# Kernel optimization log

Hardware: AMD Instinct MI355X
Metric: run time of the kernel (lower is better)

Reference implementation:

```python
import jax, jax.numpy as jnp
from jax import lax
import numpy as np

KERNEL = 3      # patch kernel
RATE = 2        # dilation / downscale rate
SCALE = 10.0    # softmax_scale
EPS = 1e-4


def extract_patches(x, k, s):
    """TF tf.image.extract_patches with SAME padding.
    x: [B,H,W,C] -> [B, oh, ow, k, k, C] with (ky,kx,c) ordering like TF depth."""
    B, H, W, C = x.shape
    oh, ow = -(-H // s), -(-W // s)
    ph = max((oh - 1) * s + k - H, 0)
    pw = max((ow - 1) * s + k - W, 0)
    xp = jnp.pad(x, ((0, 0), (ph // 2, ph - ph // 2), (pw // 2, pw - pw // 2), (0, 0)))
    rows = []
    for ky in range(k):
        cols = [xp[:, ky: ky + (oh - 1) * s + 1: s, kx: kx + (ow - 1) * s + 1: s, :]
                for kx in range(k)]
        rows.append(jnp.stack(cols, axis=3))        # [B,oh,ow,kx,C]
    return jnp.stack(rows, axis=3)                  # [B,oh,ow,ky,kx,C]


def resize_half(x):
    B, H, W, C = x.shape
    return jax.image.resize(x, (B, H // 2, W // 2, C), 'bilinear', antialias=False)


def fuse_diag(a):
    """conv2d of [N,N] image with eye(3) kernel (SAME): out[i,j]=a[i-1,j-1]+a[i,j]+a[i+1,j+1]."""
    p = jnp.pad(a, 1)
    return p[:-2, :-2] + p[1:-1, 1:-1] + p[2:, 2:]


def setup_inputs() -> dict:
    key = jax.random.key(0)
    x = jax.random.normal(key, (4, 96, 96, 128), jnp.float32)
    # binary mask with a central square hole (1 = missing region)
    mask = jnp.zeros((4, 96, 96, 1), jnp.float32).at[:, 24:72, 24:72, :].set(1.0)
    return {"x": x, "mask": mask}


def reference(x, mask):
    B, H, W, C = x.shape
    k, rate = KERNEL, RATE

    # raw patches from full-res x, stride rate -> deconv weights
    raw_p = extract_patches(x, k, rate)                     # [B,h,w,k,k,C]
    h, w = raw_p.shape[1], raw_p.shape[2]
    L = h * w
    raw_w = raw_p.reshape(B, L, k, k, C).transpose(0, 2, 3, 4, 1)   # [B,k,k,C,L]

    # downscaled foreground/background (f == b in this module) and mask
    f = resize_half(x)                                      # [B,h,w,C]
    m = resize_half(mask)                                   # [B,h,w,1]

    wp = extract_patches(f, k, 1).reshape(B, L, k, k, C).transpose(0, 2, 3, 4, 1)  # [B,k,k,C,L]
    mp = extract_patches(m, k, 1).reshape(B, L, -1)         # [B,L,k*k*1]
    mm = (jnp.mean(mp, axis=-1) == 0.0).astype(x.dtype)     # [B,L] valid-patch mask

    fp = extract_patches(f, k, 1)                           # [B,h,w,k,k,C] query patches

    def per_sample(fp_i, wi, raw_wi, mm_i):
        # normalized cross-correlation: conv2d(f_i, wi_normed, SAME)
        norm = jnp.maximum(jnp.sqrt(jnp.sum(wi * wi, axis=(0, 1, 2))), EPS)   # [L]
        wn = wi / norm
        yi = jnp.einsum('hwabc,abcl->hwl', fp_i, wn)        # [h,w,L]

        # diagonal fuse (eye(3) conv) on both patch-grid orderings
        a = fuse_diag(yi.reshape(L, L))
        a = a.reshape(h, w, h, w).transpose(1, 0, 3, 2).reshape(L, L)
        a = fuse_diag(a)
        a = a.reshape(w, h, w, h).transpose(1, 0, 3, 2)     # [h,w,h,w]
        yi = a.reshape(h, w, L)

        # masked softmax over source patches
        yi = yi * mm_i
        yi = jax.nn.softmax(yi * SCALE, axis=-1) * mm_i

        # conv2d_transpose(yi, raw_wi, [1,H,W,C], strides=rate) == vjp of strided conv
        def fwd(z):  # z: [H,W,C] -> [h,w,L]
            return lax.conv_general_dilated(z[None], raw_wi, (rate, rate), 'SAME',
                                            dimension_numbers=('NHWC', 'HWIO', 'NHWC'))[0]
        _, vjp = jax.vjp(fwd, jnp.zeros((H, W, C), x.dtype))
        return vjp(yi)[0] / (rate * rate)                   # [H,W,C]

    return jax.vmap(per_sample)(fp, wp, raw_w, mm)          # [B,H,W,C]
```

## Files before the change

kernel.cpp:

```cpp
#include <hip/hip_runtime.h>
#include <hip/hip_fp16.h>
#include <stdint.h>
#include <string.h>


namespace {

constexpr int B_ = 4;
constexpr int H_ = 96;
constexpr int W_ = 96;
constexpr int C_ = 128;
constexpr int h_ = 48;
constexpr int L_ = 2304;
constexpr int N9_ = 1152;
constexpr int K3_ = 384;
constexpr float SCALE_ = 10.0f;
constexpr float EPS_ = 1e-4f;

constexpr int OUT_F16 = 1;
constexpr int OUT_BF16 = 2;

typedef unsigned short u16;
typedef __attribute__((ext_vector_type(8))) short bfrag8;
typedef __attribute__((ext_vector_type(8))) unsigned short ushort8;
typedef __attribute__((ext_vector_type(4))) float f32x4;
typedef __attribute__((ext_vector_type(2))) float f32x2;

__device__ __forceinline__ u16 f2bf(float f) {
  uint32_t x;
  __builtin_memcpy(&x, &f, 4);
  uint32_t lsb = (x >> 16) & 1u;
  x += 0x7fffu + lsb;
  return (u16)(x >> 16);
}
__device__ __forceinline__ float bf2f(u16 u) {
  uint32_t v = ((uint32_t)u) << 16;
  float f;
  __builtin_memcpy(&f, &v, 4);
  return f;
}
__device__ __forceinline__ u16 f2h(float f) {
  __half h = __float2half(f);
  u16 u;
  __builtin_memcpy(&u, &h, 2);
  return u;
}
__device__ __forceinline__ float h2f(u16 u) {
  __half h;
  __builtin_memcpy(&h, &u, 2);
  return __half2float(h);
}

__device__ __forceinline__ void gload16(const u16* g, void* l) {
  __builtin_amdgcn_global_load_lds(
      (const __attribute__((address_space(1))) void*)g,
      (__attribute__((address_space(3))) void*)l, 16, 0, 0);
}

__device__ __forceinline__ int xcd_swz8(int orig, int nwg) {
  int q = nwg >> 3, r = nwg & 7;
  int xcd = orig & 7, pos = orig >> 3;
  return (xcd < r ? xcd * (q + 1) : r * (q + 1) + (xcd - r) * q) + pos;
}

__device__ __forceinline__ uint32_t swzb(uint32_t byte) {
  return byte ^ (((byte >> 7) & 7u) << 4);
}

__global__ __launch_bounds__(128) void k_down(const float* __restrict__ x,
                                              u16* __restrict__ F3a,
                                              u16* __restrict__ F3b,
                                              float* __restrict__ S) {
  int blk = blockIdx.x;
  int b = blk / L_, l = blk % L_;
  int p = l / h_, q = l % h_;
  int c = threadIdx.x;
  const float* xb = x + (((size_t)b * H_ + 2 * p) * W_ + 2 * q) * C_ + c;
  float v = 0.25f * (xb[0] + xb[C_] + xb[(size_t)W_ * C_] + xb[(size_t)W_ * C_ + C_]);
  u16 hi = f2bf(v);
  u16 lo = f2bf(v - bf2f(hi));
  size_t base = ((size_t)b * L_ + l) * K3_;
  F3a[base + c] = hi; F3a[base + 128 + c] = hi; F3a[base + 256 + c] = lo;
  F3b[base + c] = hi; F3b[base + 128 + c] = lo; F3b[base + 256 + c] = hi;
  float ss = v * v;
#pragma unroll
  for (int o = 32; o >= 1; o >>= 1) ss += __shfl_xor(ss, o, 64);
  __shared__ float w2[2];
  if ((c & 63) == 0) w2[c >> 6] = ss;
  __syncthreads();
  if (c == 0) S[(size_t)b * L_ + l] = w2[0] + w2[1];
}

__global__ __launch_bounds__(256) void k_mask(const float* __restrict__ mask,
                                              float* __restrict__ md) {
  int i = blockIdx.x * 256 + threadIdx.x;
  int b = i / L_, l = i % L_, p = l / h_, q = l % h_;
  const float* mb = mask + ((size_t)b * H_ + 2 * p) * W_ + 2 * q;
  md[i] = 0.25f * (mb[0] + mb[1] + mb[W_] + mb[W_ + 1]);
}

__global__ __launch_bounds__(256) void k_mmnorm(const float* __restrict__ S,
                                                const float* __restrict__ md,
                                                float* __restrict__ mm,
                                                float* __restrict__ ninv) {
  int i = blockIdx.x * 256 + threadIdx.x;
  int b = i / L_, l = i % L_, p = l / h_, q = l % h_;
  float ssum = 0.f, msum = 0.f;
#pragma unroll
  for (int a = 0; a < 3; a++) {
    int rp = p - 1 + a;
#pragma unroll
    for (int bb = 0; bb < 3; bb++) {
      int rq = q - 1 + bb;
      bool ok = ((unsigned)rp < (unsigned)h_) && ((unsigned)rq < (unsigned)h_);
      int idx = ok ? (b * L_ + rp * h_ + rq) : 0;
      float sv = S[idx], mv = md[idx];
      if (ok) { ssum += sv; msum += mv; }
    }
  }
  mm[i] = (msum == 0.f) ? 1.f : 0.f;
  float n = fmaxf(sqrtf(ssum), EPS_);
  ninv[i] = 1.f / n;
}

__global__ __launch_bounds__(256) void k_xpack(const float* __restrict__ x,
                                               u16* __restrict__ XpT) {
  int lt = blockIdx.x * 32, jt = blockIdx.y * 64, bz = blockIdx.z;
  __shared__ u16 tile[32][65];
  int t = threadIdx.x;
  int jj = t & 63, lq = t >> 6;
  for (int pass = 0; pass < 8; ++pass) {
    int ll = pass * 4 + lq;
    int l = lt + ll;
    int p = l / h_, q = l % h_;
    int j = jt + jj;
    int a = j / 384, rem = j % 384, bb = rem / 128, c = rem % 128;
    int gy = 2 * p + a, gx = 2 * q + bb;
    float v = 0.f;
    if (gy < H_ && gx < W_) v = x[(((size_t)bz * H_ + gy) * W_ + gx) * C_ + c];
    tile[ll][jj] = f2bf(v);
  }
  __syncthreads();
  int lw = t & 31, jq = t >> 5;
  for (int pass = 0; pass < 8; ++pass) {
    int j2 = pass * 8 + jq;
    XpT[((size_t)bz * N9_ + jt + j2) * L_ + lt + lw] = tile[lw][j2];
  }
}

template <int OUT>
__global__ __launch_bounds__(256) void gemm_bt(const u16* __restrict__ A,
                                               const u16* __restrict__ B,
                                               void* __restrict__ Cv,
                                               int N, int Kd,
                                               size_t sA, size_t sB, size_t sC) {
  const u16* Ab = A + (size_t)blockIdx.z * sA;
  const u16* Bb = B + (size_t)blockIdx.z * sB;
  int nwg = gridDim.x * gridDim.y;
  int orig = blockIdx.y * gridDim.x + blockIdx.x;
  int wgid = xcd_swz8(orig, nwg);
  int bx = wgid % gridDim.x, by = wgid / gridDim.x;
  int m0 = by * 128, n0 = bx * 128;

  __shared__ char As[2][8192];
  __shared__ char Bs[2][8192];
  int t = threadIdx.x;
  int lane = t & 63, wv = t >> 6, wr = wv >> 1, wc = wv & 1;
  int mrow = lane & 15, kg = lane >> 4;
  f32x4 acc[4][4];
#pragma unroll
  for (int i = 0; i < 4; i++)
#pragma unroll
    for (int j = 0; j < 4; j++) acc[i][j] = (f32x4)(0.0f);

  uint32_t d16 = (uint32_t)t * 16u;
  uint32_t sz = swzb(d16);
  int rowp = (int)(sz >> 6);
  int kcp = (int)((sz >> 4) & 3u);
  const u16* ga0 = Ab + (size_t)(m0 + rowp) * Kd + kcp * 8;
  const u16* ga1 = Ab + (size_t)(m0 + 64 + rowp) * Kd + kcp * 8;
  const u16* gb0 = Bb + (size_t)(n0 + rowp) * Kd + kcp * 8;
  const u16* gb1 = Bb + (size_t)(n0 + 64 + rowp) * Kd + kcp * 8;

  auto STAGE = [&](int buf, int k0) {
    gload16(ga0 + k0, As[buf] + wv * 1024);
    gload16(ga1 + k0, As[buf] + 4096 + wv * 1024);
    gload16(gb0 + k0, Bs[buf] + wv * 1024);
    gload16(gb1 + k0, Bs[buf] + 4096 + wv * 1024);
  };

  int nsteps = Kd >> 5;
  STAGE(0, 0);
  __syncthreads();
  int cur = 0;
  for (int s = 0; s < nsteps; ++s) {
    if (s + 1 < nsteps) STAGE(cur ^ 1, (s + 1) << 5);
    bfrag8 af[4], bf[4];
#pragma unroll
    for (int i = 0; i < 4; i++) {
      uint32_t byte = (uint32_t)(wr * 64 + i * 16 + mrow) * 64u + (uint32_t)kg * 16u;
      af[i] = *(const bfrag8*)(As[cur] + swzb(byte));
    }
#pragma unroll
    for (int i = 0; i < 4; i++) {
      uint32_t byte = (uint32_t)(wc * 64 + i * 16 + mrow) * 64u + (uint32_t)kg * 16u;
      bf[i] = *(const bfrag8*)(Bs[cur] + swzb(byte));
    }
#pragma unroll
    for (int i = 0; i < 4; i++)
#pragma unroll
      for (int j = 0; j < 4; j++)
        acc[i][j] = __builtin_amdgcn_mfma_f32_16x16x32_bf16(af[i], bf[j], acc[i][j], 0, 0, 0);
    __syncthreads();
    cur ^= 1;
  }
#pragma unroll
  for (int i = 0; i < 4; i++)
#pragma unroll
    for (int j = 0; j < 4; j++)
#pragma unroll
      for (int r = 0; r < 4; r++) {
        int gr = m0 + wr * 64 + i * 16 + kg * 4 + r;
        int gc = n0 + wc * 64 + j * 16 + mrow;
        if (OUT == OUT_BF16) {
          ((u16*)Cv)[(size_t)blockIdx.z * sC + (size_t)gr * N + gc] = f2bf(acc[i][j][r]);
        } else {
          ((u16*)Cv)[(size_t)blockIdx.z * sC + (size_t)gr * N + gc] = f2h(acc[i][j][r]);
        }
      }
}

template <int S>
__device__ __forceinline__ void tap(const u16* __restrict__ Ub, int o8, bool tok,
                                    const bool* md, int b, float* acc) {
  constexpr int REM = ((S % 8) + 8) % 8;
  int off = tok ? (o8 + S * 2305) : (8 + REM);
  float v[8];
  if constexpr (REM == 0) {
    ushort8 w = *(const ushort8*)(Ub + off);
#pragma unroll
    for (int i = 0; i < 8; i++) v[i] = h2f(w[i]);
  } else if constexpr (REM == 1) {
    ushort8 w = *(const ushort8*)(Ub + off - 1);
    u16 sc = Ub[off + 7];
#pragma unroll
    for (int i = 0; i < 7; i++) v[i] = h2f(w[i + 1]);
    v[7] = h2f(sc);
  } else {
    u16 sc = Ub[off];
    ushort8 w = *(const ushort8*)(Ub + off + 1);
    v[0] = h2f(sc);
#pragma unroll
    for (int i = 1; i < 8; i++) v[i] = h2f(w[i - 1]);
  }
#pragma unroll
  for (int i = 0; i < 8; i++) acc[i] += (tok && md[b + i]) ? v[i] : 0.f;
}

__global__ __launch_bounds__(256) void k_patchsum(const u16* __restrict__ U,
                                                  u16* __restrict__ V,
                                                  const float* __restrict__ ninv,
                                                  int b0) {
  int blk = xcd_swz8(blockIdx.x, gridDim.x);
  int bz = blockIdx.z;
  int o8 = (blk * 256 + (int)threadIdx.x) * 8;
  int R = o8 / L_;
  int col = o8 - R * L_;
  const u16* Ub = U + (size_t)bz * L_ * L_;
  u16* Vb = V + (size_t)bz * L_ * L_;
  int hq = R / h_, wq = R % h_, ps = col / h_, qs0 = col % h_;
  bool ra[3], rb[3], ca[3];
#pragma unroll
  for (int a = 0; a < 3; a++) {
    ra[a] = (unsigned)(hq - 1 + a) < (unsigned)h_;
    rb[a] = (unsigned)(wq - 1 + a) < (unsigned)h_;
    ca[a] = (unsigned)(ps - 1 + a) < (unsigned)h_;
  }
  bool md[10];
#pragma unroll
  for (int d = 0; d < 10; d++) md[d] = (unsigned)(qs0 - 1 + d) < (unsigned)h_;

  float acc[8];
#pragma unroll
  for (int i = 0; i < 8; i++) acc[i] = 0.f;

  bool t0 = ra[0] && ca[0];
  bool t1 = ra[1] && ca[1];
  bool t2 = ra[2] && ca[2];
  tap<-49>(Ub, o8, t0 && rb[0], md, 0, acc);
  tap<-48>(Ub, o8, t0 && rb[1], md, 1, acc);
  tap<-47>(Ub, o8, t0 && rb[2], md, 2, acc);
  tap<-1>(Ub, o8, t1 && rb[0], md, 0, acc);
  tap<0>(Ub, o8, t1 && rb[1], md, 1, acc);
  tap<1>(Ub, o8, t1 && rb[2], md, 2, acc);
  tap<47>(Ub, o8, t2 && rb[0], md, 0, acc);
  tap<48>(Ub, o8, t2 && rb[1], md, 1, acc);
  tap<49>(Ub, o8, t2 && rb[2], md, 2, acc);

  const float* nvb = ninv + (size_t)(b0 + bz) * L_ + col;
  ushort8 ov;
#pragma unroll
  for (int i = 0; i < 8; i++) ov[i] = f2h(acc[i] * nvb[i]);
  *(ushort8*)(Vb + o8) = ov;
}

__global__ __launch_bounds__(256) void k_fsm(const u16* __restrict__ V1,
                                             const float* __restrict__ mm,
                                             u16* __restrict__ Aout,
                                             int b0) {
  int i = xcd_swz8(blockIdx.x, L_), bz = blockIdx.y;
  int hq = i / h_, wq = i % h_;
  const u16* Vb = V1 + (size_t)bz * L_ * L_;
  const float* mmb = mm + (size_t)(b0 + bz) * L_;
  u16* arow = Aout + ((size_t)bz * L_ + i) * L_;
  int t = threadIdx.x;

  uint32_t rowBase[3];
  bool rw0[3], rw1[3], rw2[3];
#pragma unroll
  for (int d2 = 0; d2 < 3; d2++) {
    int TA = wq * h_ + hq + (d2 - 1);
    bool ok = (TA >= 0) && (TA < L_);
    int TAc = ok ? TA : 0;
    int iB = (TAc % h_) * h_ + TAc / h_;
    rowBase[d2] = (uint32_t)(iB * L_);
    rw0[d2] = ok && (iB - 1 >= 0);
    rw1[d2] = ok;
    rw2[d2] = ok && (iB + 1 < L_);
  }

  int jy = t / h_, jx = t % h_;
  float y[9];
  float mx = -3.0e38f;
#pragma unroll
  for (int cc = 0; cc < 9; cc++) {
    int j = cc * 256 + t;
    int jB0 = (jy >= 1) ? (j - h_) : (j + (L_ - h_ - 1));
    int jB1 = j;
    int jB2 = (jy <= h_ - 2) ? (j + h_) : (j - (L_ - h_ - 1));
    bool tb0 = (j > 0), tb2 = (j < L_ - 1);
    float s = 0.f;
    {
      uint32_t oc = rowBase[0] + (uint32_t)jB0;
      bool w0 = rw0[0] && tb0 && (jB0 > 0);
      bool w1 = rw1[0] && tb0;
      bool w2 = rw2[0] && tb0 && (jB0 < L_ - 1);
      float vm = h2f(Vb[w0 ? oc - (L_ + 1) : 0u]);
      float vc = h2f(Vb[w1 ? oc : 0u]);
      float vp = h2f(Vb[w2 ? oc + (L_ + 1) : 0u]);
      s += (w0 ? vm : 0.f) + (w1 ? vc : 0.f) + (w2 ? vp : 0.f);
    }
    {
      uint32_t oc = rowBase[1] + (uint32_t)jB1;
      bool w0 = rw0[1] && (jB1 > 0);
      bool w1 = rw1[1];
      bool w2 = rw2[1] && (jB1 < L_ - 1);
      float vm = h2f(Vb[w0 ? oc - (L_ + 1) : 0u]);
      float vc = h2f(Vb[w1 ? oc : 0u]);
      float vp = h2f(Vb[w2 ? oc + (L_ + 1) : 0u]);
      s += (w0 ? vm : 0.f) + (w1 ? vc : 0.f) + (w2 ? vp : 0.f);
    }
    {
      uint32_t oc = rowBase[2] + (uint32_t)jB2;
      bool w0 = rw0[2] && tb2 && (jB2 > 0);
      bool w1 = rw1[2] && tb2;
      bool w2 = rw2[2] && tb2 && (jB2 < L_ - 1);
      float vm = h2f(Vb[w0 ? oc - (L_ + 1) : 0u]);
      float vc = h2f(Vb[w1 ? oc : 0u]);
      float vp = h2f(Vb[w2 ? oc + (L_ + 1) : 0u]);
      s += (w0 ? vm : 0.f) + (w1 ? vc : 0.f) + (w2 ? vp : 0.f);
    }
    float zv = s * mmb[j] * SCALE_;
    y[cc] = zv;
    mx = fmaxf(mx, zv);
    jx += 256 - 5 * h_;
    jy += 5;
    if (jx >= h_) { jx -= h_; jy += 1; }
  }

  int lane = t & 63, wid = t >> 6;
  __shared__ float wredm[4];
  __shared__ float wreds[4];
#pragma unroll
  for (int o = 32; o >= 1; o >>= 1) mx = fmaxf(mx, __shfl_xor(mx, o, 64));
  if (lane == 0) wredm[wid] = mx;
  __syncthreads();
  float MX = fmaxf(fmaxf(wredm[0], wredm[1]), fmaxf(wredm[2], wredm[3]));
  float sm = 0.f;
#pragma unroll
  for (int cc = 0; cc < 9; cc++) {
    y[cc] = __expf(y[cc] - MX);
    sm += y[cc];
  }
#pragma unroll
  for (int o = 32; o >= 1; o >>= 1) sm += __shfl_xor(sm, o, 64);
  if (lane == 0) wreds[wid] = sm;
  __syncthreads();
  float inv = 1.0f / (wreds[0] + wreds[1] + wreds[2] + wreds[3]);
#pragma unroll
  for (int cc = 0; cc < 9; cc++) {
    int j = cc * 256 + t;
    arow[j] = f2bf(y[cc] * inv * mmb[j]);
  }
}

__global__ __launch_bounds__(256) void k_scatter(const u16* __restrict__ P,
                                                 float* __restrict__ out) {
  int idx = blockIdx.x * 256 + threadIdx.x;
  int c2 = idx & 63;
  int r = idx >> 6;
  int xx = r % W_; r /= W_;
  int y = r % H_;
  int bz = r / H_;
  const u16* Pb = P + (size_t)bz * L_ * N9_;
  int yo[2], ya[2], ny = 0;
  if (y & 1) { yo[0] = y >> 1; ya[0] = 1; ny = 1; }
  else {
    yo[0] = y >> 1; ya[0] = 0; ny = 1;
    if (y >= 2) { yo[1] = (y >> 1) - 1; ya[1] = 2; ny = 2; }
  }
  int xo[2], xa[2], nx = 0;
  if (xx & 1) { xo[0] = xx >> 1; xa[0] = 1; nx = 1; }
  else {
    xo[0] = xx >> 1; xa[0] = 0; nx = 1;
    if (xx >= 2) { xo[1] = (xx >> 1) - 1; xa[1] = 2; nx = 2; }
  }
  float s0 = 0.f, s1 = 0.f;
  for (int i = 0; i < ny; i++)
    for (int j = 0; j < nx; j++) {
      size_t off = (size_t)(yo[i] * h_ + xo[j]) * N9_ + (ya[i] * 3 + xa[j]) * C_ + 2 * c2;
      uint32_t w = *(const uint32_t*)(Pb + off);
      s0 += bf2f((u16)(w & 0xffffu));
      s1 += bf2f((u16)(w >> 16));
    }
  f32x2 o;
  o[0] = 0.25f * s0;
  o[1] = 0.25f * s1;
  *(f32x2*)(out + ((size_t)bz * H_ + y) * (size_t)W_ * C_ + (size_t)xx * C_ + 2 * c2) = o;
}

}

extern "C" void kernel_launch(void* const* d_in, const int* in_sizes, int n_in,
                              void* d_out, int out_size, void* d_ws, size_t ws_size,
                              hipStream_t stream) {
  (void)in_sizes; (void)n_in; (void)out_size;
  const float* x = (const float*)d_in[0];
  const float* mask = (const float*)d_in[1];
  float* out = (float*)d_out;
  char* ws = (char*)d_ws;

  const size_t szF3 = (size_t)B_ * L_ * K3_ * sizeof(u16);
  const size_t szSm = (size_t)B_ * L_ * sizeof(float);
  const size_t off_F3a = 0;
  const size_t off_F3b = off_F3a + szF3;
  const size_t off_S = off_F3b + szF3;
  const size_t off_md = off_S + szSm;
  const size_t off_mm = off_md + szSm;
  const size_t off_nv = off_mm + szSm;
  const size_t off_fixed_end = off_nv + szSm;

  const size_t perXp = (size_t)N9_ * L_ * sizeof(u16);
  const size_t perU = (size_t)L_ * L_ * sizeof(u16);
  const size_t perV = (size_t)L_ * L_ * sizeof(u16);
  int G = 4;
  while (G > 1 && off_fixed_end + (size_t)G * (perXp + perU + perV) > ws_size) G >>= 1;

  const size_t off_XpT = off_fixed_end;
  const size_t off_U = off_XpT + (size_t)G * perXp;
  const size_t off_V = off_U + (size_t)G * perU;

  u16* F3a = (u16*)(ws + off_F3a);
  u16* F3b = (u16*)(ws + off_F3b);
  float* S = (float*)(ws + off_S);
  float* md = (float*)(ws + off_md);
  float* mm = (float*)(ws + off_mm);
  float* nv = (float*)(ws + off_nv);
  u16* XpT = (u16*)(ws + off_XpT);
  u16* U = (u16*)(ws + off_U);
  u16* V = (u16*)(ws + off_V);
  u16* Abuf = (u16*)(ws + off_U);
  u16* Pbuf = (u16*)(ws + off_V);

  k_down<<<dim3(B_ * L_), dim3(C_), 0, stream>>>(x, F3a, F3b, S);
  k_mask<<<dim3((B_ * L_) / 256), dim3(256), 0, stream>>>(mask, md);
  k_mmnorm<<<dim3((B_ * L_) / 256), dim3(256), 0, stream>>>(S, md, mm, nv);

  for (int sb = 0; sb < B_; sb += G) {
    const float* xs = x + (size_t)sb * H_ * W_ * C_;
    k_xpack<<<dim3(L_ / 32, N9_ / 64, G), dim3(256), 0, stream>>>(xs, XpT);
    gemm_bt<OUT_F16><<<dim3(L_ / 128, L_ / 128, G), dim3(256), 0, stream>>>(
        F3a + (size_t)sb * L_ * K3_, F3b + (size_t)sb * L_ * K3_, (void*)U,
        L_, K3_, (size_t)L_ * K3_, (size_t)L_ * K3_, (size_t)L_ * L_);
    k_patchsum<<<dim3((L_ * L_) / (256 * 8), 1, G), dim3(256), 0, stream>>>(U, V, nv, sb);
    k_fsm<<<dim3(L_, G), dim3(256), 0, stream>>>(V, mm, Abuf, sb);
    gemm_bt<OUT_BF16><<<dim3(N9_ / 128, L_ / 128, G), dim3(256), 0, stream>>>(
        Abuf, XpT, (void*)Pbuf, N9_, L_,
        (size_t)L_ * L_, (size_t)N9_ * L_, (size_t)L_ * N9_);
    k_scatter<<<dim3((G * H_ * W_ * C_ / 2) / 256), dim3(256), 0, stream>>>(
        Pbuf, out + (size_t)sb * H_ * W_ * C_);
  }
}
```

Before: 204.1 us.

## Exploit symmetry of self-correlation GEMM to compute only upper-triangular tiles

The first GEMM multiplies F3a by F3b^T, and both are built from the same downscaled input, so the L×L correlation matrix is treated as symmetric. The launch now covers only the 171 upper-triangular 128×128 tiles of the 18×18 tile grid instead of all 324. Each off-diagonal tile also writes its transpose with packed 4-element stores. This roughly halves the MFMA work and input loads of that GEMM. In exchange the mirrored stores are strided, the tile index is decoded with a small loop, and correctness depends on F3a·F3b^T really being symmetric.

Result: faster. 197.4 us (-3.3%).

```diff
diff --git a/kernel.cpp b/kernel.cpp
--- a/kernel.cpp
+++ b/kernel.cpp
@@ -23,6 +23,7 @@
 typedef unsigned short u16;
 typedef __attribute__((ext_vector_type(8))) short bfrag8;
 typedef __attribute__((ext_vector_type(8))) unsigned short ushort8;
+typedef __attribute__((ext_vector_type(4))) unsigned short ushort4v;
 typedef __attribute__((ext_vector_type(4))) float f32x4;
 typedef __attribute__((ext_vector_type(2))) float f32x2;
 
@@ -148,7 +149,7 @@
   }
 }
 
-template <int OUT>
+template <int OUT, bool SYMM>
 __global__ __launch_bounds__(256) void gemm_bt(const u16* __restrict__ A,
                                                const u16* __restrict__ B,
                                                void* __restrict__ Cv,
@@ -156,10 +157,20 @@
                                                size_t sA, size_t sB, size_t sC) {
   const u16* Ab = A + (size_t)blockIdx.z * sA;
   const u16* Bb = B + (size_t)blockIdx.z * sB;
-  int nwg = gridDim.x * gridDim.y;
-  int orig = blockIdx.y * gridDim.x + blockIdx.x;
-  int wgid = xcd_swz8(orig, nwg);
-  int bx = wgid % gridDim.x, by = wgid / gridDim.x;
+  int bx, by;
+  if (SYMM) {
+    int wgid = xcd_swz8(blockIdx.x, gridDim.x);
+    int t2 = wgid, row = 0, len = 18;
+    while (t2 >= len) { t2 -= len; --len; ++row; }
+    by = row;
+    bx = row + t2;
+  } else {
+    int nwg = gridDim.x * gridDim.y;
+    int orig = blockIdx.y * gridDim.x + blockIdx.x;
+    int wgid = xcd_swz8(orig, nwg);
+    bx = wgid % gridDim.x;
+    by = wgid / gridDim.x;
+  }
   int m0 = by * 128, n0 = bx * 128;
 
   __shared__ char As[2][8192];
@@ -228,6 +239,20 @@
           ((u16*)Cv)[(size_t)blockIdx.z * sC + (size_t)gr * N + gc] = f2h(acc[i][j][r]);
         }
       }
+  if (SYMM && bx > by) {
+    u16* Cb = (u16*)Cv + (size_t)blockIdx.z * sC;
+#pragma unroll
+    for (int i = 0; i < 4; i++)
+#pragma unroll
+      for (int j = 0; j < 4; j++) {
+        int grb = m0 + wr * 64 + i * 16 + kg * 4;
+        int gc = n0 + wc * 64 + j * 16 + mrow;
+        ushort4v pk;
+#pragma unroll
+        for (int r = 0; r < 4; r++) pk[r] = f2h(acc[i][j][r]);
+        *(ushort4v*)(Cb + (size_t)gc * N + grb) = pk;
+      }
+  }
 }
 
 template <int S>
@@ -489,12 +514,12 @@
   for (int sb = 0; sb < B_; sb += G) {
     const float* xs = x + (size_t)sb * H_ * W_ * C_;
     k_xpack<<<dim3(L_ / 32, N9_ / 64, G), dim3(256), 0, stream>>>(xs, XpT);
-    gemm_bt<OUT_F16><<<dim3(L_ / 128, L_ / 128, G), dim3(256), 0, stream>>>(
+    gemm_bt<OUT_F16, true><<<dim3(171, 1, G), dim3(256), 0, stream>>>(
         F3a + (size_t)sb * L_ * K3_, F3b + (size_t)sb * L_ * K3_, (void*)U,
         L_, K3_, (size_t)L_ * K3_, (size_t)L_ * K3_, (size_t)L_ * L_);
     k_patchsum<<<dim3((L_ * L_) / (256 * 8), 1, G), dim3(256), 0, stream>>>(U, V, nv, sb);
     k_fsm<<<dim3(L_, G), dim3(256), 0, stream>>>(V, mm, Abuf, sb);
-    gemm_bt<OUT_BF16><<<dim3(N9_ / 128, L_ / 128, G), dim3(256), 0, stream>>>(
+    gemm_bt<OUT_BF16, false><<<dim3(N9_ / 128, L_ / 128, G), dim3(256), 0, stream>>>(
         Abuf, XpT, (void*)Pbuf, N9_, L_,
         (size_t)L_ * L_, (size_t)N9_ * L_, (size_t)L_ * N9_);
     k_scatter<<<dim3((G * H_ * W_ * C_ / 2) / 256), dim3(256), 0, stream>>>(
```
